# Kernel tuning notes

Measured on AMD Instinct MI355X. Metric: run time of the kernel, lower is better.

Reference implementation:

```python
import jax, jax.numpy as jnp
import numpy as np

BRANCH = 16   # children per internal node
DEPTH = 4     # levels 0..4, leaves at level 4
IN = 512
HID = 512

def _level_sizes():
    return [BRANCH ** d for d in range(DEPTH + 1)]

def setup_inputs() -> dict:
    key = jax.random.key(0)
    ks = jax.random.split(key, 9)
    N = sum(_level_sizes())  # 69905
    x = jax.random.normal(ks[0], (N, IN), dtype=jnp.float32)
    s = 1.0 / np.sqrt(IN + HID)  # torch nn.Linear default init bound
    def lin(kw, kb):
        w = jax.random.uniform(kw, (HID, IN + HID), jnp.float32, -s, s)
        b = jax.random.uniform(kb, (HID,), jnp.float32, -s, s)
        return w, b
    wi_w, wi_b = lin(ks[1], ks[2])
    wf_w, wf_b = lin(ks[3], ks[4])
    wo_w, wo_b = lin(ks[5], ks[6])
    wu_w, wu_b = lin(ks[7], ks[8])
    return {"x": x, "wi_w": wi_w, "wi_b": wi_b, "wf_w": wf_w, "wf_b": wf_b,
            "wo_w": wo_w, "wo_b": wo_b, "wu_w": wu_w, "wu_b": wu_b}

def reference(x, wi_w, wi_b, wf_w, wf_b, wo_w, wo_b, wu_w, wu_b):
    sizes = _level_sizes()
    offs = np.concatenate([[0], np.cumsum(sizes)])
    levels = [x[offs[d]:offs[d + 1]] for d in range(DEPTH + 1)]

    def gates(xh):
        i = jax.nn.sigmoid(xh @ wi_w.T + wi_b)
        o = jax.nn.sigmoid(xh @ wo_w.T + wo_b)
        u = jnp.tanh(xh @ wu_w.T + wu_b)
        return i, o, u

    # leaf_forward: h_prev = 0, no forget terms
    Xl = levels[DEPTH]
    xh = jnp.concatenate([Xl, jnp.zeros((Xl.shape[0], HID), Xl.dtype)], axis=1)
    i, o, u = gates(xh)
    C = i * u
    H = o * jnp.tanh(C)

    # node_forward, bottom-up. Faithful quirk of the source: the forget gate
    # is computed on the child CELL state (cat(x, c_k)), not the hidden state.
    for d in range(DEPTH - 1, -1, -1):
        Xd = levels[d]                      # [n, IN]
        n = Xd.shape[0]
        Hc = H.reshape(n, BRANCH, HID)      # children hidden
        Cc = C.reshape(n, BRANCH, HID)      # children cell
        h_sum = Hc.sum(axis=1)
        xh = jnp.concatenate([Xd, h_sum], axis=1)
        i, o, u = gates(xh)
        xc = jnp.concatenate([jnp.broadcast_to(Xd[:, None, :], (n, BRANCH, IN)), Cc], axis=-1)
        f = jax.nn.sigmoid(jnp.einsum('nbk,hk->nbh', xc, wf_w) + wf_b)
        C = i * u + (f * Cc).sum(axis=1)
        H = o * jnp.tanh(C)

    return H[0], C[0]
```

## Files before the change

### kernel.cpp

```cpp
#include <hip/hip_runtime.h>
#include <stdint.h>
#include <stddef.h>


typedef __bf16 bf16x8 __attribute__((ext_vector_type(8)));
typedef float  f32x4  __attribute__((ext_vector_type(4)));
typedef void __attribute__((address_space(3))) lds_void_t;
typedef void __attribute__((address_space(1))) gbl_void_t;

__device__ __forceinline__ uint16_t f2bf(float f) {
  union { __bf16 b; uint16_t u; } v;
  v.b = (__bf16)f;
  return v.u;
}
__device__ __forceinline__ float bf2f(uint16_t u) {
  union { uint32_t u; float f; } v; v.u = (uint32_t)u << 16;
  return v.f;
}
__device__ __forceinline__ float sig_(float x) {
  return __builtin_amdgcn_rcpf(1.0f + __expf(-x));
}
__device__ __forceinline__ float tanh_(float x) {
  return __builtin_fmaf(2.f,
      __builtin_amdgcn_rcpf(1.f + __expf(-2.f * x)), -1.f);
}

__global__ void k_conv_all(const float4* __restrict__ x,
                           ushort4* __restrict__ xdst, long n4x,
                           const float4* __restrict__ w0,
                           const float4* __restrict__ w1,
                           const float4* __restrict__ w2,
                           const float4* __restrict__ w3,
                           ushort4* __restrict__ wdst) {
  const long per4 = (long)512 * 1024 / 4;
  const long total = n4x + 4 * per4;
  long i = blockIdx.x * (long)blockDim.x + threadIdx.x;
  long stride = (long)gridDim.x * blockDim.x;
  for (; i < total; i += stride) {
    float4 v;
    ushort4* d;
    if (i < n4x) {
      v = x[i];
      d = xdst + i;
    } else {
      long j = i - n4x;
      long seg = j / per4, off2 = j - seg * per4;
      const float4* s = (seg == 0) ? w0 : (seg == 1) ? w1
                       : (seg == 2) ? w2 : w3;
      v = s[off2];
      d = wdst + j;
    }
    ushort4 r;
    r.x = f2bf(v.x); r.y = f2bf(v.y); r.z = f2bf(v.z); r.w = f2bf(v.w);
    *d = r;
  }
}

#define BM 128
#define BN 128
#define BK 32

__global__ __launch_bounds__(256)
void k_gemm_bt(const uint16_t* __restrict__ A, int lda,
               const uint16_t* __restrict__ B, int ldb,
               float* __restrict__ C, int ldc, int K) {
  __shared__ uint16_t As[BM * BK];
  __shared__ uint16_t Bs[BN * BK];
  const int tid = threadIdx.x, lane = tid & 63, wave = tid >> 6;
  const int lrow = lane & 15, quad = lane >> 4;
  const int wm = (wave >> 1) * 64, wn = (wave & 1) * 64;
  const long tm = blockIdx.x, tn = blockIdx.y;
  f32x4 acc[4][4] = {};
  const int srow = lane >> 2, scol = (lane & 3) * 8;
  for (int k0 = 0; k0 < K; k0 += BK) {
#pragma unroll
    for (int i = 0; i < 2; ++i) {
      int row = i * 64 + wave * 16 + srow;
      const uint16_t* gp = A + (tm * BM + row) * (long)lda + k0 + scol;
      __builtin_amdgcn_global_load_lds((gbl_void_t*)(uintptr_t)gp,
          (lds_void_t*)&As[i * 2048 + wave * 512], 16, 0, 0);
    }
#pragma unroll
    for (int i = 0; i < 2; ++i) {
      int row = i * 64 + wave * 16 + srow;
      const uint16_t* gp = B + (tn * BN + row) * (long)ldb + k0 + scol;
      __builtin_amdgcn_global_load_lds((gbl_void_t*)(uintptr_t)gp,
          (lds_void_t*)&Bs[i * 2048 + wave * 512], 16, 0, 0);
    }
    __syncthreads();
    bf16x8 a[4], b[4];
#pragma unroll
    for (int f = 0; f < 4; ++f)
      a[f] = *(const bf16x8*)&As[(wm + f * 16 + lrow) * BK + quad * 8];
#pragma unroll
    for (int f = 0; f < 4; ++f)
      b[f] = *(const bf16x8*)&Bs[(wn + f * 16 + lrow) * BK + quad * 8];
#pragma unroll
    for (int fm = 0; fm < 4; ++fm)
#pragma unroll
      for (int fn = 0; fn < 4; ++fn)
        acc[fm][fn] = __builtin_amdgcn_mfma_f32_16x16x32_bf16(
            a[fm], b[fn], acc[fm][fn], 0, 0, 0);
    __syncthreads();
  }
#pragma unroll
  for (int fm = 0; fm < 4; ++fm)
#pragma unroll
    for (int fn = 0; fn < 4; ++fn) {
      long col  = tn * BN + wn + fn * 16 + lrow;
      long row0 = tm * BM + wm + fm * 16 + quad * 4;
#pragma unroll
      for (int r = 0; r < 4; ++r)
        C[(row0 + r) * (long)ldc + col] = acc[fm][fn][r];
    }
}

template <bool HAS_F, int MF>
__global__ __launch_bounds__(256, 3)
void k_level(const uint16_t* __restrict__ A, int lda, int K,
             const uint16_t* __restrict__ Wg,
             const float* __restrict__ bi, const float* __restrict__ bo,
             const float* __restrict__ bu,
             const float* __restrict__ Fpart,
             uint16_t* __restrict__ Cbf,
             const uint16_t* __restrict__ Xnext,
             uint16_t* __restrict__ xh_next) {
  constexpr int BMT = MF * 32;
  __shared__ uint16_t As[BMT * 64];
  __shared__ uint16_t Bs[192 * 64];
  const int tid = threadIdx.x, lane = tid & 63, wave = tid >> 6;
  const int lrow = lane & 15, quad = lane >> 4;
  const int wm = (wave >> 1) * (MF * 16), wn = (wave & 1) * 32;

  long tm, tn;
  {
    const int nTm = (int)(gridDim.x >> 3);
    int b = blockIdx.x;
    if ((nTm & 7) == 0) {
      int x = b & 7, j = b >> 3, per = nTm >> 3;
      tn = j & 7; tm = (long)x * per + (j >> 3);
    } else { tm = b >> 3; tn = b & 7; }
  }

  f32x4 acc[3][MF][2] = {};

  const int srow = lane >> 3;
  const int scol = (((lane & 7) ^ srow) << 3);
  const int rsw = lrow & 7;
  const int pc[2] = { ((0 + quad) ^ rsw) << 3, ((4 + quad) ^ rsw) << 3 };

  for (int k0 = 0; k0 < K; k0 += 64) {
#pragma unroll
    for (int j = 0; j < MF; ++j) {
      int grp = wave * MF + j;
      int row = grp * 8 + srow;
      const uint16_t* gp = A + (tm * BMT + row) * (long)lda + k0 + scol;
      __builtin_amdgcn_global_load_lds((gbl_void_t*)(uintptr_t)gp,
          (lds_void_t*)&As[grp * 512], 16, 0, 0);
    }
#pragma unroll
    for (int j = 0; j < 6; ++j) {
      int cc = wave * 6 + j;
      int g  = cc >> 3;
      long grow = (long)g * 512 + tn * 64 + (cc & 7) * 8 + srow;
      const uint16_t* gp = Wg + grow * 1024 + k0 + scol;
      __builtin_amdgcn_global_load_lds((gbl_void_t*)(uintptr_t)gp,
          (lds_void_t*)&Bs[cc * 512], 16, 0, 0);
    }
    __syncthreads();

#pragma unroll
    for (int h = 0; h < 2; ++h) {
      bf16x8 a[MF];
#pragma unroll
      for (int f = 0; f < MF; ++f)
        a[f] = *(const bf16x8*)&As[(wm + f * 16 + lrow) * 64 + pc[h]];
#pragma unroll
      for (int g = 0; g < 3; ++g) {
        bf16x8 b0 = *(const bf16x8*)&Bs[(g * 64 + wn + lrow) * 64 + pc[h]];
        bf16x8 b1 = *(const bf16x8*)&Bs[(g * 64 + wn + 16 + lrow) * 64 +
                                        pc[h]];
#pragma unroll
        for (int fm = 0; fm < MF; ++fm) {
          acc[g][fm][0] = __builtin_amdgcn_mfma_f32_16x16x32_bf16(
              a[fm], b0, acc[g][fm][0], 0, 0, 0);
          acc[g][fm][1] = __builtin_amdgcn_mfma_f32_16x16x32_bf16(
              a[fm], b1, acc[g][fm][1], 0, 0, 0);
        }
      }
    }
    __syncthreads();
  }

#pragma unroll
  for (int fn = 0; fn < 2; ++fn) {
    long col = tn * 64 + wn + fn * 16 + lrow;
    float biv = bi[col], bov = bo[col], buv = bu[col];
#pragma unroll
    for (int fm = 0; fm < MF; ++fm) {
      long row0 = tm * BMT + wm + fm * 16 + quad * 4;
      long pg   = tm * (BMT / 16) + (wm >> 4) + fm;
      float hs = 0.f;
#pragma unroll
      for (int r = 0; r < 4; ++r) {
        long row = row0 + r;
        float iv = sig_(acc[0][fm][fn][r] + biv);
        float ov = sig_(acc[1][fm][fn][r] + bov);
        float uv = tanh_(acc[2][fm][fn][r] + buv);
        float c  = iv * uv;
        if (HAS_F) c += Fpart[row * 512 + col];
        Cbf[row * 512 + col] = f2bf(c);
        hs += ov * tanh_(c);
      }
      hs += __shfl_xor(hs, 16, 64);
      hs += __shfl_xor(hs, 32, 64);
      if (quad == 0) {
        xh_next[pg * 1024 + col]       = Xnext[pg * 512 + col];
        xh_next[pg * 1024 + 512 + col] = f2bf(hs);
      }
    }
  }
}

template <int MF>
__global__ __launch_bounds__(256, 3)
void k_fc_combine(const uint16_t* __restrict__ Cbf,
                  const uint16_t* __restrict__ Wfc, int ldb,
                  const float* __restrict__ Fx,
                  const float* __restrict__ bfb,
                  float* __restrict__ Fpart) {
  constexpr int BMT = MF * 32;
  __shared__ uint16_t As[BMT * 64];
  __shared__ uint16_t Bs[128 * 64];
  const int tid = threadIdx.x, lane = tid & 63, wave = tid >> 6;
  const int lrow = lane & 15, quad = lane >> 4;
  const int wm = (wave >> 1) * (MF * 16), wn = (wave & 1) * 64;
  long tm, tn;
  {
    const int nTm = (int)(gridDim.x >> 2);
    int b = blockIdx.x;
    if ((nTm & 7) == 0) {
      int x = b & 7, j = b >> 3, per = nTm >> 3;
      tn = j & 3; tm = (long)x * per + (j >> 2);
    } else { tm = b >> 2; tn = b & 3; }
  }
  const int lda = 512;
  f32x4 acc[MF][4] = {};

  const int srow = lane >> 3;
  const int scol = (((lane & 7) ^ srow) << 3);
  const int rsw = lrow & 7;
  const int pc[2] = { ((0 + quad) ^ rsw) << 3, ((4 + quad) ^ rsw) << 3 };

  for (int k0 = 0; k0 < 512; k0 += 64) {
#pragma unroll
    for (int j = 0; j < MF; ++j) {
      int grp = wave * MF + j;
      int row = grp * 8 + srow;
      const uint16_t* gp = Cbf + (tm * BMT + row) * (long)lda + k0 + scol;
      __builtin_amdgcn_global_load_lds((gbl_void_t*)(uintptr_t)gp,
          (lds_void_t*)&As[grp * 512], 16, 0, 0);
    }
#pragma unroll
    for (int j = 0; j < 4; ++j) {
      int row = wave * 32 + j * 8 + srow;
      const uint16_t* gp = Wfc + (tn * BN + row) * (long)ldb + k0 + scol;
      __builtin_amdgcn_global_load_lds((gbl_void_t*)(uintptr_t)gp,
          (lds_void_t*)&Bs[(wave * 32 + j * 8) * 64], 16, 0, 0);
    }
    __syncthreads();
#pragma unroll
    for (int h = 0; h < 2; ++h) {
      bf16x8 a[MF], b[4];
#pragma unroll
      for (int f = 0; f < MF; ++f)
        a[f] = *(const bf16x8*)&As[(wm + f * 16 + lrow) * 64 + pc[h]];
#pragma unroll
      for (int f = 0; f < 4; ++f)
        b[f] = *(const bf16x8*)&Bs[(wn + f * 16 + lrow) * 64 + pc[h]];
#pragma unroll
      for (int fm = 0; fm < MF; ++fm)
#pragma unroll
        for (int fn = 0; fn < 4; ++fn)
          acc[fm][fn] = __builtin_amdgcn_mfma_f32_16x16x32_bf16(
              a[fm], b[fn], acc[fm][fn], 0, 0, 0);
    }
    __syncthreads();
  }
#pragma unroll
  for (int fm = 0; fm < MF; ++fm) {
    long pg   = tm * (BMT / 16) + (wm >> 4) + fm;
    long row0 = tm * BMT + wm + fm * 16 + quad * 4;
#pragma unroll
    for (int fn = 0; fn < 4; ++fn) {
      long col = tn * BN + wn + fn * 16 + lrow;
      float fx = Fx[pg * 512 + col] + bfb[col];
      float t = 0.f;
#pragma unroll
      for (int r = 0; r < 4; ++r)
        t += sig_(fx + acc[fm][fn][r]) * bf2f(Cbf[(row0 + r) * 512 + col]);
      t += __shfl_xor(t, 16, 64);
      t += __shfl_xor(t, 32, 64);
      if (quad == 0) Fpart[pg * 512 + col] = t;
    }
  }
}

__global__ void k_dot_bb(const uint16_t* __restrict__ A, int lda,
                         const uint16_t* __restrict__ B, int ldb,
                         float* __restrict__ C, int ldc,
                         int M, int N, int K) {
  int wid  = (int)((blockIdx.x * (long)blockDim.x + threadIdx.x) >> 6);
  int lane = threadIdx.x & 63;
  if (wid >= M * N) return;
  int m = wid / N, n = wid - m * N;
  const uint16_t* a = A + (long)m * lda;
  const uint16_t* b = B + (long)n * ldb;
  int per = K >> 6, k0 = lane * per;
  float s = 0.f;
  for (int j = 0; j < per; j += 4) {
    ushort4 av = *(const ushort4*)(a + k0 + j);
    ushort4 bv = *(const ushort4*)(b + k0 + j);
    s += bf2f(av.x) * bf2f(bv.x) + bf2f(av.y) * bf2f(bv.y)
       + bf2f(av.z) * bf2f(bv.z) + bf2f(av.w) * bf2f(bv.w);
  }
#pragma unroll
  for (int off = 32; off; off >>= 1) s += __shfl_xor(s, off, 64);
  if (lane == 0) C[(long)m * ldc + n] = s;
}

__global__ void k_dot_merge(const uint16_t* __restrict__ xhC,
                            const uint16_t* __restrict__ Wg,
                            float* __restrict__ Gf,
                            const float* __restrict__ CupA,
                            const float* __restrict__ WfF,
                            float* __restrict__ Fc) {
  int wid  = (int)((blockIdx.x * (long)blockDim.x + threadIdx.x) >> 6);
  int lane = threadIdx.x & 63;
  if (wid < 1536) {
    const uint16_t* a = xhC;
    const uint16_t* b = Wg + (long)wid * 1024;
    int k0 = lane * 16;
    float s = 0.f;
#pragma unroll
    for (int j = 0; j < 16; j += 4) {
      ushort4 av = *(const ushort4*)(a + k0 + j);
      ushort4 bv = *(const ushort4*)(b + k0 + j);
      s += bf2f(av.x) * bf2f(bv.x) + bf2f(av.y) * bf2f(bv.y)
         + bf2f(av.z) * bf2f(bv.z) + bf2f(av.w) * bf2f(bv.w);
    }
#pragma unroll
    for (int off = 32; off; off >>= 1) s += __shfl_xor(s, off, 64);
    if (lane == 0) Gf[wid] = s;
  } else {
    int w2 = wid - 1536;
    if (w2 >= 16 * 512) return;
    int m = w2 >> 9, n = w2 & 511;
    const float* a = CupA + (long)m * 512;
    const float* b = WfF + (long)n * 1024;
    int k0 = lane * 8;
    float s = 0.f;
#pragma unroll
    for (int j = 0; j < 8; j += 4) {
      float4 av = *(const float4*)(a + k0 + j);
      float4 bv = *(const float4*)(b + k0 + j);
      s += av.x * bv.x + av.y * bv.y + av.z * bv.z + av.w * bv.w;
    }
#pragma unroll
    for (int off = 32; off; off >>= 1) s += __shfl_xor(s, off, 64);
    if (lane == 0) Fc[(long)m * 512 + n] = s;
  }
}

__global__ __launch_bounds__(1024)
void k_lvl1_tail(const float* __restrict__ G,
                 const float* __restrict__ Fpart,
                 const float* __restrict__ bi,
                 const float* __restrict__ bo,
                 const float* __restrict__ bu,
                 float* __restrict__ Cv,
                 const uint16_t* __restrict__ xroot,
                 uint16_t* __restrict__ xh) {
  __shared__ float Hl[16 * 512];
  const int tid = threadIdx.x;
#pragma unroll
  for (int it = 0; it < 2; ++it) {
    int idx = it * 1024 + tid;
    int p = idx >> 7, hq = (idx & 127) << 2;
    const float* g = G + (long)p * 1536;
    float4 gi = *(const float4*)(g + hq);
    float4 go = *(const float4*)(g + 512 + hq);
    float4 gu = *(const float4*)(g + 1024 + hq);
    float4 b_i = *(const float4*)(bi + hq);
    float4 b_o = *(const float4*)(bo + hq);
    float4 b_u = *(const float4*)(bu + hq);
    float4 fp = *(const float4*)(Fpart + (long)p * 512 + hq);
    const float* gip = &gi.x; const float* gop = &go.x;
    const float* gup = &gu.x; const float* bip = &b_i.x;
    const float* bop = &b_o.x; const float* bup = &b_u.x;
    const float* fpp = &fp.x;
    float4 hv, cv;
    float* hvp = &hv.x; float* cvp = &cv.x;
#pragma unroll
    for (int j = 0; j < 4; ++j) {
      float iv = sig_(gip[j] + bip[j]);
      float ov = sig_(gop[j] + bop[j]);
      float uv = tanh_(gup[j] + bup[j]);
      float c  = iv * uv + fpp[j];
      cvp[j] = c;
      hvp[j] = ov * tanh_(c);
    }
    *(float4*)(Cv + (long)p * 512 + hq) = cv;
    *(float4*)(&Hl[p * 512 + hq]) = hv;
  }
  __syncthreads();
  if (tid < 128) {
    int hq = tid << 2;
    float4 s = {0.f, 0.f, 0.f, 0.f};
#pragma unroll
    for (int b = 0; b < 16; ++b) {
      float4 v = *(const float4*)(&Hl[b * 512 + hq]);
      s.x += v.x; s.y += v.y; s.z += v.z; s.w += v.w;
    }
    *(ushort4*)(xh + hq) = *(const ushort4*)(xroot + hq);
    ushort4 hw = {f2bf(s.x), f2bf(s.y), f2bf(s.z), f2bf(s.w)};
    *(ushort4*)(xh + 512 + hq) = hw;
  }
}

__global__ void k_root_tail(const float* __restrict__ Fc,
                            const float* __restrict__ Fx,
                            const float* __restrict__ bfb,
                            const float* __restrict__ Cc,
                            const float* __restrict__ G,
                            const float* __restrict__ bi,
                            const float* __restrict__ bo,
                            const float* __restrict__ bu,
                            float* __restrict__ H, float* __restrict__ Cv) {
  int hq = (threadIdx.x & 127) << 2;
  float4 fxv = *(const float4*)(Fx + hq);
  float4 bfv = *(const float4*)(bfb + hq);
  float fx0 = fxv.x + bfv.x, fx1 = fxv.y + bfv.y;
  float fx2 = fxv.z + bfv.z, fx3 = fxv.w + bfv.w;
  float a0 = 0.f, a1 = 0.f, a2 = 0.f, a3 = 0.f;
#pragma unroll 4
  for (int b = 0; b < 16; ++b) {
    float4 f = *(const float4*)(Fc + (long)b * 512 + hq);
    float4 c = *(const float4*)(Cc + (long)b * 512 + hq);
    a0 += sig_(fx0 + f.x) * c.x;
    a1 += sig_(fx1 + f.y) * c.y;
    a2 += sig_(fx2 + f.z) * c.z;
    a3 += sig_(fx3 + f.w) * c.w;
  }
  float fpp[4] = {a0, a1, a2, a3};
  float4 gi = *(const float4*)(G + hq);
  float4 go = *(const float4*)(G + 512 + hq);
  float4 gu = *(const float4*)(G + 1024 + hq);
  float4 b_i = *(const float4*)(bi + hq);
  float4 b_o = *(const float4*)(bo + hq);
  float4 b_u = *(const float4*)(bu + hq);
  const float* gip = &gi.x; const float* gop = &go.x; const float* gup = &gu.x;
  const float* bip = &b_i.x; const float* bop = &b_o.x; const float* bup = &b_u.x;
  float4 hv, cv;
  float* hvp = &hv.x; float* cvp = &cv.x;
#pragma unroll
  for (int j = 0; j < 4; ++j) {
    float iv = sig_(gip[j] + bip[j]);
    float ov = sig_(gop[j] + bop[j]);
    float uv = tanh_(gup[j] + bup[j]);
    float c  = iv * uv + fpp[j];
    cvp[j] = c;
    hvp[j] = ov * tanh_(c);
  }
  *(float4*)(H  + hq) = hv;
  *(float4*)(Cv + hq) = cv;
}

extern "C" void kernel_launch(void* const* d_in, const int* in_sizes, int n_in,
                              void* d_out, int out_size, void* d_ws, size_t ws_size,
                              hipStream_t stream) {
  const float* x    = (const float*)d_in[0];
  const float* wi_w = (const float*)d_in[1];
  const float* wi_b = (const float*)d_in[2];
  const float* wf_w = (const float*)d_in[3];
  const float* wf_b = (const float*)d_in[4];
  const float* wo_w = (const float*)d_in[5];
  const float* wo_b = (const float*)d_in[6];
  const float* wu_w = (const float*)d_in[7];
  const float* wu_b = (const float*)d_in[8];
  (void)in_sizes; (void)n_in; (void)out_size; (void)ws_size;

  static const long offs[5] = {0, 1, 17, 273, 4369};
  const long NTOT = 69905;

  char* ws = (char*)d_ws;
  size_t off = 0;
  auto alloc = [&](size_t bytes) -> void* {
    void* p = ws + off;
    off += (bytes + 255) & ~(size_t)255;
    return p;
  };
  uint16_t* Xbf   = (uint16_t*)alloc(NTOT * 512 * 2);
  uint16_t* Wgw   = (uint16_t*)alloc((size_t)2048 * 1024 * 2);
  uint16_t* Wg    = Wgw;
  uint16_t* Wf    = Wgw + (size_t)1536 * 1024;
  float*    FxAll = (float*)alloc((size_t)4480 * 512 * 4);
  uint16_t* Cbf   = (uint16_t*)alloc((size_t)65536 * 512 * 2);
  uint16_t* CbfU  = (uint16_t*)alloc((size_t)4096 * 512 * 2);
  uint16_t* CbfU2 = (uint16_t*)alloc((size_t)256 * 512 * 2);
  uint16_t* xhA   = (uint16_t*)alloc((size_t)4096 * 1024 * 2);
  uint16_t* xhB   = (uint16_t*)alloc((size_t)256 * 1024 * 2);
  uint16_t* xhC   = (uint16_t*)alloc((size_t)16 * 1024 * 2);
  float*    Fpart = (float*)alloc((size_t)4096 * 512 * 4);
  float*    Gf    = (float*)alloc((size_t)16 * 1536 * 4);
  float*    Fc    = (float*)alloc((size_t)16 * 512 * 4);
  float*    CupA  = (float*)alloc((size_t)16 * 512 * 4);

  {
    long n4x = NTOT * 512 / 4;
    k_conv_all<<<8192, 256, 0, stream>>>(
        (const float4*)x, (ushort4*)Xbf, n4x,
        (const float4*)wi_w, (const float4*)wo_w,
        (const float4*)wu_w, (const float4*)wf_w, (ushort4*)Wgw);
  }

  {
    dim3 grid(35, 4);
    k_gemm_bt<<<grid, 256, 0, stream>>>(Xbf, 512, Wf, 1024, FxAll, 512, 512);
  }

  k_level<false, 4><<<4096, 256, 0, stream>>>(
      Xbf + offs[4] * 512, 512, 512, Wg, wi_b, wo_b, wu_b, nullptr,
      Cbf, Xbf + offs[3] * 512, xhA);
  k_fc_combine<4><<<2048, 256, 0, stream>>>(Cbf, Wf + 512, 1024,
                                            FxAll + offs[3] * 512, wf_b, Fpart);

  k_level<true, 2><<<512, 256, 0, stream>>>(
      xhA, 1024, 1024, Wg, wi_b, wo_b, wu_b, Fpart,
      CbfU, Xbf + offs[2] * 512, xhB);
  k_fc_combine<2><<<256, 256, 0, stream>>>(CbfU, Wf + 512, 1024,
                                           FxAll + offs[2] * 512, wf_b, Fpart);

  k_level<true, 2><<<32, 256, 0, stream>>>(
      xhB, 1024, 1024, Wg, wi_b, wo_b, wu_b, Fpart,
      CbfU2, Xbf + offs[1] * 512, xhC);
  k_fc_combine<2><<<16, 256, 0, stream>>>(CbfU2, Wf + 512, 1024,
                                          FxAll + offs[1] * 512, wf_b, Fpart);

  {
    long waves = 16L * 1536;
    k_dot_bb<<<(int)((waves * 64 + 255) / 256), 256, 0, stream>>>(
        xhC, 1024, Wg, 1024, Gf, 1536, 16, 1536, 1024);
    k_lvl1_tail<<<1, 1024, 0, stream>>>(Gf, Fpart, wi_b, wo_b, wu_b,
                                        CupA, Xbf + offs[0] * 512, xhC);
  }

  {
    long waves = 1536 + 16L * 512;
    k_dot_merge<<<(int)(waves / 4), 256, 0, stream>>>(
        xhC, Wg, Gf, CupA, wf_w + 512, Fc);
  }
  k_root_tail<<<1, 128, 0, stream>>>(Fc, FxAll, wf_b, CupA, Gf,
                                     wi_b, wo_b, wu_b,
                                     (float*)d_out, (float*)d_out + 512);
}
```

Before: 494.9 us.

## Merge leaf gates with Fx GEMM, and fc_combine with dot_bb, into shared launches

The leaf-level gate GEMM is rewritten as a dedicated kernel with 64-wide K tiles and swizzled LDS. It shares one launch with the Fx projection GEMM: the extra blocks beyond 4096 compute FxAll. Separately, the level-1 forget-combine and the small dot-product kernel are merged into one launch via a block-index split. The aim is to remove launch overhead and the serialization of independent kernels on the stream, so the small tail kernels can overlap with other blocks. In exchange, register and LDS usage is shared across heterogeneous branches, which may cut occupancy.

Measured after the change: 471.8 us. -4.7%, faster.

```diff
diff --git a/kernel.cpp b/kernel.cpp
--- a/kernel.cpp
+++ b/kernel.cpp
@@ -60,59 +60,156 @@
 #define BN 128
 #define BK 32
 
-__global__ __launch_bounds__(256)
-void k_gemm_bt(const uint16_t* __restrict__ A, int lda,
-               const uint16_t* __restrict__ B, int ldb,
-               float* __restrict__ C, int ldc, int K) {
-  __shared__ uint16_t As[BM * BK];
-  __shared__ uint16_t Bs[BN * BK];
+__global__ __launch_bounds__(256, 3)
+void k_leaf_fx(const uint16_t* __restrict__ Xleaf,
+               const uint16_t* __restrict__ Wg,
+               const float* __restrict__ bi, const float* __restrict__ bo,
+               const float* __restrict__ bu,
+               uint16_t* __restrict__ Cbf,
+               const uint16_t* __restrict__ Xnext,
+               uint16_t* __restrict__ xh_next,
+               const uint16_t* __restrict__ Xbf,
+               const uint16_t* __restrict__ Wf,
+               float* __restrict__ FxAll) {
+  __shared__ uint16_t smem[20480];
   const int tid = threadIdx.x, lane = tid & 63, wave = tid >> 6;
   const int lrow = lane & 15, quad = lane >> 4;
-  const int wm = (wave >> 1) * 64, wn = (wave & 1) * 64;
-  const long tm = blockIdx.x, tn = blockIdx.y;
-  f32x4 acc[4][4] = {};
-  const int srow = lane >> 2, scol = (lane & 3) * 8;
-  for (int k0 = 0; k0 < K; k0 += BK) {
-#pragma unroll
-    for (int i = 0; i < 2; ++i) {
-      int row = i * 64 + wave * 16 + srow;
-      const uint16_t* gp = A + (tm * BM + row) * (long)lda + k0 + scol;
-      __builtin_amdgcn_global_load_lds((gbl_void_t*)(uintptr_t)gp,
-          (lds_void_t*)&As[i * 2048 + wave * 512], 16, 0, 0);
-    }
-#pragma unroll
-    for (int i = 0; i < 2; ++i) {
-      int row = i * 64 + wave * 16 + srow;
-      const uint16_t* gp = B + (tn * BN + row) * (long)ldb + k0 + scol;
-      __builtin_amdgcn_global_load_lds((gbl_void_t*)(uintptr_t)gp,
-          (lds_void_t*)&Bs[i * 2048 + wave * 512], 16, 0, 0);
-    }
-    __syncthreads();
-    bf16x8 a[4], b[4];
-#pragma unroll
-    for (int f = 0; f < 4; ++f)
-      a[f] = *(const bf16x8*)&As[(wm + f * 16 + lrow) * BK + quad * 8];
-#pragma unroll
-    for (int f = 0; f < 4; ++f)
-      b[f] = *(const bf16x8*)&Bs[(wn + f * 16 + lrow) * BK + quad * 8];
+
+  if (blockIdx.x < 4096) {
+    uint16_t* As = smem;
+    uint16_t* Bs = smem + 8192;
+    const int wm = (wave >> 1) * 64, wn = (wave & 1) * 32;
+    long tm, tn;
+    {
+      const int nTm = 512;
+      int b = blockIdx.x;
+      int x = b & 7, j = b >> 3, per = nTm >> 3;
+      tn = j & 7; tm = (long)x * per + (j >> 3);
+    }
+    f32x4 acc[3][4][2] = {};
+    const int srow = lane >> 3;
+    const int scol = (((lane & 7) ^ srow) << 3);
+    const int rsw = lrow & 7;
+    const int pc[2] = { ((0 + quad) ^ rsw) << 3, ((4 + quad) ^ rsw) << 3 };
+
+    for (int k0 = 0; k0 < 512; k0 += 64) {
+#pragma unroll
+      for (int j = 0; j < 4; ++j) {
+        int grp = wave * 4 + j;
+        int row = grp * 8 + srow;
+        const uint16_t* gp = Xleaf + (tm * 128 + row) * 512L + k0 + scol;
+        __builtin_amdgcn_global_load_lds((gbl_void_t*)(uintptr_t)gp,
+            (lds_void_t*)&As[grp * 512], 16, 0, 0);
+      }
+#pragma unroll
+      for (int j = 0; j < 6; ++j) {
+        int cc = wave * 6 + j;
+        int g  = cc >> 3;
+        long grow = (long)g * 512 + tn * 64 + (cc & 7) * 8 + srow;
+        const uint16_t* gp = Wg + grow * 1024 + k0 + scol;
+        __builtin_amdgcn_global_load_lds((gbl_void_t*)(uintptr_t)gp,
+            (lds_void_t*)&Bs[cc * 512], 16, 0, 0);
+      }
+      __syncthreads();
+#pragma unroll
+      for (int h = 0; h < 2; ++h) {
+        bf16x8 a[4];
+#pragma unroll
+        for (int f = 0; f < 4; ++f)
+          a[f] = *(const bf16x8*)&As[(wm + f * 16 + lrow) * 64 + pc[h]];
+#pragma unroll
+        for (int g = 0; g < 3; ++g) {
+          bf16x8 b0 = *(const bf16x8*)&Bs[(g * 64 + wn + lrow) * 64 + pc[h]];
+          bf16x8 b1 = *(const bf16x8*)&Bs[(g * 64 + wn + 16 + lrow) * 64 +
+                                          pc[h]];
+#pragma unroll
+          for (int fm = 0; fm < 4; ++fm) {
+            acc[g][fm][0] = __builtin_amdgcn_mfma_f32_16x16x32_bf16(
+                a[fm], b0, acc[g][fm][0], 0, 0, 0);
+            acc[g][fm][1] = __builtin_amdgcn_mfma_f32_16x16x32_bf16(
+                a[fm], b1, acc[g][fm][1], 0, 0, 0);
+          }
+        }
+      }
+      __syncthreads();
+    }
+#pragma unroll
+    for (int fn = 0; fn < 2; ++fn) {
+      long col = tn * 64 + wn + fn * 16 + lrow;
+      float biv = bi[col], bov = bo[col], buv = bu[col];
+#pragma unroll
+      for (int fm = 0; fm < 4; ++fm) {
+        long row0 = tm * 128 + wm + fm * 16 + quad * 4;
+        long pg   = tm * 8 + (wm >> 4) + fm;
+        float hs = 0.f;
+#pragma unroll
+        for (int r = 0; r < 4; ++r) {
+          long row = row0 + r;
+          float iv = sig_(acc[0][fm][fn][r] + biv);
+          float ov = sig_(acc[1][fm][fn][r] + bov);
+          float uv = tanh_(acc[2][fm][fn][r] + buv);
+          float c  = iv * uv;
+          Cbf[row * 512 + col] = f2bf(c);
+          hs += ov * tanh_(c);
+        }
+        hs += __shfl_xor(hs, 16, 64);
+        hs += __shfl_xor(hs, 32, 64);
+        if (quad == 0) {
+          xh_next[pg * 1024 + col]       = Xnext[pg * 512 + col];
+          xh_next[pg * 1024 + 512 + col] = f2bf(hs);
+        }
+      }
+    }
+  } else {
+    uint16_t* As = smem;
+    uint16_t* Bs = smem + 4096;
+    const int wm = (wave >> 1) * 64, wn = (wave & 1) * 64;
+    int bid2 = (int)blockIdx.x - 4096;
+    const long tm = bid2 % 35, tn = bid2 / 35;
+    f32x4 acc[4][4] = {};
+    const int srow2 = lane >> 2, scol2 = (lane & 3) * 8;
+    for (int k0 = 0; k0 < 512; k0 += BK) {
+#pragma unroll
+      for (int i = 0; i < 2; ++i) {
+        int row = i * 64 + wave * 16 + srow2;
+        const uint16_t* gp = Xbf + (tm * BM + row) * 512L + k0 + scol2;
+        __builtin_amdgcn_global_load_lds((gbl_void_t*)(uintptr_t)gp,
+            (lds_void_t*)&As[i * 2048 + wave * 512], 16, 0, 0);
+      }
+#pragma unroll
+      for (int i = 0; i < 2; ++i) {
+        int row = i * 64 + wave * 16 + srow2;
+        const uint16_t* gp = Wf + (tn * BN + row) * 1024L + k0 + scol2;
+        __builtin_amdgcn_global_load_lds((gbl_void_t*)(uintptr_t)gp,
+            (lds_void_t*)&Bs[i * 2048 + wave * 512], 16, 0, 0);
+      }
+      __syncthreads();
+      bf16x8 a[4], b[4];
+#pragma unroll
+      for (int f = 0; f < 4; ++f)
+        a[f] = *(const bf16x8*)&As[(wm + f * 16 + lrow) * BK + quad * 8];
+#pragma unroll
+      for (int f = 0; f < 4; ++f)
+        b[f] = *(const bf16x8*)&Bs[(wn + f * 16 + lrow) * BK + quad * 8];
+#pragma unroll
+      for (int fm = 0; fm < 4; ++fm)
+#pragma unroll
+        for (int fn = 0; fn < 4; ++fn)
+          acc[fm][fn] = __builtin_amdgcn_mfma_f32_16x16x32_bf16(
+              a[fm], b[fn], acc[fm][fn], 0, 0, 0);
+      __syncthreads();
+    }
 #pragma unroll
     for (int fm = 0; fm < 4; ++fm)
 #pragma unroll
-      for (int fn = 0; fn < 4; ++fn)
-        acc[fm][fn] = __builtin_amdgcn_mfma_f32_16x16x32_bf16(
-            a[fm], b[fn], acc[fm][fn], 0, 0, 0);
-    __syncthreads();
-  }
-#pragma unroll
-  for (int fm = 0; fm < 4; ++fm)
-#pragma unroll
-    for (int fn = 0; fn < 4; ++fn) {
-      long col  = tn * BN + wn + fn * 16 + lrow;
-      long row0 = tm * BM + wm + fm * 16 + quad * 4;
-#pragma unroll
-      for (int r = 0; r < 4; ++r)
-        C[(row0 + r) * (long)ldc + col] = acc[fm][fn][r];
-    }
+      for (int fn = 0; fn < 4; ++fn) {
+        long col  = tn * BN + wn + fn * 16 + lrow;
+        long row0 = tm * BM + wm + fm * 16 + quad * 4;
+#pragma unroll
+        for (int r = 0; r < 4; ++r)
+          FxAll[(row0 + r) * 512 + col] = acc[fm][fn][r];
+      }
+  }
 }
 
 template <bool HAS_F, int MF>
@@ -306,27 +403,100 @@
   }
 }
 
-__global__ void k_dot_bb(const uint16_t* __restrict__ A, int lda,
-                         const uint16_t* __restrict__ B, int ldb,
-                         float* __restrict__ C, int ldc,
-                         int M, int N, int K) {
-  int wid  = (int)((blockIdx.x * (long)blockDim.x + threadIdx.x) >> 6);
-  int lane = threadIdx.x & 63;
-  if (wid >= M * N) return;
-  int m = wid / N, n = wid - m * N;
-  const uint16_t* a = A + (long)m * lda;
-  const uint16_t* b = B + (long)n * ldb;
-  int per = K >> 6, k0 = lane * per;
-  float s = 0.f;
-  for (int j = 0; j < per; j += 4) {
-    ushort4 av = *(const ushort4*)(a + k0 + j);
-    ushort4 bv = *(const ushort4*)(b + k0 + j);
-    s += bf2f(av.x) * bf2f(bv.x) + bf2f(av.y) * bf2f(bv.y)
-       + bf2f(av.z) * bf2f(bv.z) + bf2f(av.w) * bf2f(bv.w);
-  }
-#pragma unroll
-  for (int off = 32; off; off >>= 1) s += __shfl_xor(s, off, 64);
-  if (lane == 0) C[(long)m * ldc + n] = s;
+__global__ __launch_bounds__(256)
+void k_fcdot(const uint16_t* __restrict__ Cbf,
+             const uint16_t* __restrict__ Wfc,
+             const float* __restrict__ Fx,
+             const float* __restrict__ bfb,
+             float* __restrict__ Fpart,
+             const uint16_t* __restrict__ xhC,
+             const uint16_t* __restrict__ Wg,
+             float* __restrict__ Gf) {
+  __shared__ uint16_t smem[12288];
+  const int tid = threadIdx.x, lane = tid & 63, wave = tid >> 6;
+  if (blockIdx.x < 16) {
+    uint16_t* As = smem;
+    uint16_t* Bs = smem + 4096;
+    const int lrow = lane & 15, quad = lane >> 4;
+    const int wm = (wave >> 1) * 32, wn = (wave & 1) * 64;
+    int b = blockIdx.x;
+    long tm = b >> 2, tn = b & 3;
+    f32x4 acc[2][4] = {};
+    const int srow = lane >> 3;
+    const int scol = (((lane & 7) ^ srow) << 3);
+    const int rsw = lrow & 7;
+    const int pc[2] = { ((0 + quad) ^ rsw) << 3, ((4 + quad) ^ rsw) << 3 };
+    for (int k0 = 0; k0 < 512; k0 += 64) {
+#pragma unroll
+      for (int j = 0; j < 2; ++j) {
+        int grp = wave * 2 + j;
+        int row = grp * 8 + srow;
+        const uint16_t* gp = Cbf + (tm * 64 + row) * 512L + k0 + scol;
+        __builtin_amdgcn_global_load_lds((gbl_void_t*)(uintptr_t)gp,
+            (lds_void_t*)&As[grp * 512], 16, 0, 0);
+      }
+#pragma unroll
+      for (int j = 0; j < 4; ++j) {
+        int row = wave * 32 + j * 8 + srow;
+        const uint16_t* gp = Wfc + (tn * 128 + row) * 1024L + k0 + scol;
+        __builtin_amdgcn_global_load_lds((gbl_void_t*)(uintptr_t)gp,
+            (lds_void_t*)&Bs[(wave * 32 + j * 8) * 64], 16, 0, 0);
+      }
+      __syncthreads();
+#pragma unroll
+      for (int h = 0; h < 2; ++h) {
+        bf16x8 a[2], bb[4];
+#pragma unroll
+        for (int f = 0; f < 2; ++f)
+          a[f] = *(const bf16x8*)&As[(wm + f * 16 + lrow) * 64 + pc[h]];
+#pragma unroll
+        for (int f = 0; f < 4; ++f)
+          bb[f] = *(const bf16x8*)&Bs[(wn + f * 16 + lrow) * 64 + pc[h]];
+#pragma unroll
+        for (int fm = 0; fm < 2; ++fm)
+#pragma unroll
+          for (int fn = 0; fn < 4; ++fn)
+            acc[fm][fn] = __builtin_amdgcn_mfma_f32_16x16x32_bf16(
+                a[fm], bb[fn], acc[fm][fn], 0, 0, 0);
+      }
+      __syncthreads();
+    }
+#pragma unroll
+    for (int fm = 0; fm < 2; ++fm) {
+      long pg   = tm * 4 + (wm >> 4) + fm;
+      long row0 = tm * 64 + wm + fm * 16 + quad * 4;
+#pragma unroll
+      for (int fn = 0; fn < 4; ++fn) {
+        long col = tn * 128 + wn + fn * 16 + lrow;
+        float fx = Fx[pg * 512 + col] + bfb[col];
+        float t = 0.f;
+#pragma unroll
+        for (int r = 0; r < 4; ++r)
+          t += sig_(fx + acc[fm][fn][r]) * bf2f(Cbf[(row0 + r) * 512 + col]);
+        t += __shfl_xor(t, 16, 64);
+        t += __shfl_xor(t, 32, 64);
+        if (quad == 0) Fpart[pg * 512 + col] = t;
+      }
+    }
+  } else {
+    int wid = (int)(((long)(blockIdx.x - 16) * 256 + tid) >> 6);
+    if (wid >= 16 * 1536) return;
+    int m = wid / 1536, n = wid - m * 1536;
+    const uint16_t* a = xhC + (long)m * 1024;
+    const uint16_t* b = Wg + (long)n * 1024;
+    int k0 = lane * 16;
+    float s = 0.f;
+#pragma unroll
+    for (int j = 0; j < 16; j += 4) {
+      ushort4 av = *(const ushort4*)(a + k0 + j);
+      ushort4 bv = *(const ushort4*)(b + k0 + j);
+      s += bf2f(av.x) * bf2f(bv.x) + bf2f(av.y) * bf2f(bv.y)
+         + bf2f(av.z) * bf2f(bv.z) + bf2f(av.w) * bf2f(bv.w);
+    }
+#pragma unroll
+    for (int off = 32; off; off >>= 1) s += __shfl_xor(s, off, 64);
+    if (lane == 0) Gf[(long)m * 1536 + n] = s;
+  }
 }
 
 __global__ void k_dot_merge(const uint16_t* __restrict__ xhC,
@@ -524,14 +694,10 @@
         (const float4*)wu_w, (const float4*)wf_w, (ushort4*)Wgw);
   }
 
-  {
-    dim3 grid(35, 4);
-    k_gemm_bt<<<grid, 256, 0, stream>>>(Xbf, 512, Wf, 1024, FxAll, 512, 512);
-  }
-
-  k_level<false, 4><<<4096, 256, 0, stream>>>(
-      Xbf + offs[4] * 512, 512, 512, Wg, wi_b, wo_b, wu_b, nullptr,
-      Cbf, Xbf + offs[3] * 512, xhA);
+  k_leaf_fx<<<4236, 256, 0, stream>>>(
+      Xbf + offs[4] * 512, Wg, wi_b, wo_b, wu_b,
+      Cbf, Xbf + offs[3] * 512, xhA,
+      Xbf, Wf, FxAll);
   k_fc_combine<4><<<2048, 256, 0, stream>>>(Cbf, Wf + 512, 1024,
                                             FxAll + offs[3] * 512, wf_b, Fpart);
 
@@ -544,16 +710,13 @@
   k_level<true, 2><<<32, 256, 0, stream>>>(
       xhB, 1024, 1024, Wg, wi_b, wo_b, wu_b, Fpart,
       CbfU2, Xbf + offs[1] * 512, xhC);
-  k_fc_combine<2><<<16, 256, 0, stream>>>(CbfU2, Wf + 512, 1024,
-                                          FxAll + offs[1] * 512, wf_b, Fpart);
-
-  {
-    long waves = 16L * 1536;
-    k_dot_bb<<<(int)((waves * 64 + 255) / 256), 256, 0, stream>>>(
-        xhC, 1024, Wg, 1024, Gf, 1536, 16, 1536, 1024);
-    k_lvl1_tail<<<1, 1024, 0, stream>>>(Gf, Fpart, wi_b, wo_b, wu_b,
-                                        CupA, Xbf + offs[0] * 512, xhC);
-  }
+
+  k_fcdot<<<6160, 256, 0, stream>>>(CbfU2, Wf + 512,
+                                    FxAll + offs[1] * 512, wf_b, Fpart,
+                                    xhC, Wg, Gf);
+
+  k_lvl1_tail<<<1, 1024, 0, stream>>>(Gf, Fpart, wi_b, wo_b, wu_b,
+                                      CupA, Xbf + offs[0] * 512, xhC);
 
   {
     long waves = 1536 + 16L * 512;
```
